# Optimization experiments

Measured on AMD Instinct MI355X. Metric: run time of the kernel, lower is better.

## Reference

```python
import jax, jax.numpy as jnp
import numpy as np

B, N, M = 256, 2048, 128          # batch, memory rows, memory word size
VEC, H, E = 256, 1024, 512        # vector_length, hidden_size, embed_dim
SHIFTS = 3                        # shift kernel size {-1,0,+1}
P = M + 3 + SHIFTS                # k(M), beta(1), g(1), s(3), gamma(1)
EPS = 1e-16


def _xavier(k, shape):
    fan_out, fan_in = shape
    lim = float(np.sqrt(6.0 / (fan_in + fan_out)))
    return jax.random.uniform(k, shape, jnp.float32, -lim, lim)


def setup_inputs() -> dict:
    key = jax.random.key(0)
    ks = jax.random.split(key, 16)
    x = jax.random.normal(ks[0], (B, VEC + M), jnp.float32)
    memory = jax.random.normal(ks[1], (B, N, M), jnp.float32) * 0.1
    prev_read_w = jax.nn.softmax(jax.random.normal(ks[2], (B, N), jnp.float32), axis=1)
    prev_write_w = jax.nn.softmax(jax.random.normal(ks[3], (B, N), jnp.float32), axis=1)
    h_prev = jax.random.normal(ks[4], (B, H), jnp.float32) * 0.1
    c_prev = jax.random.normal(ks[5], (B, H), jnp.float32) * 0.1
    # LSTM controller params (torch gate order i,f,g,o)
    W_ih = _xavier(ks[6], (4 * H, VEC + M))
    W_hh = _xavier(ks[7], (4 * H, H))
    b_ih = jnp.zeros((4 * H,), jnp.float32)
    b_hh = jnp.zeros((4 * H,), jnp.float32)
    # read head fc: hidden -> k,beta,g,s,gamma
    W_r = _xavier(ks[8], (P, H)); b_r = jnp.zeros((P,), jnp.float32)
    # write head fc: hidden -> k,beta,g,s,gamma,e(M),a(M)
    W_w = _xavier(ks[9], (P + 2 * M, H)); b_w = jnp.zeros((P + 2 * M,), jnp.float32)
    # output fc: (hidden + M) -> embed_dim
    W_fc = _xavier(ks[10], (E, H + M))
    b_fc = jax.random.normal(ks[11], (E,), jnp.float32) * 0.01
    return dict(x=x, memory=memory, prev_read_w=prev_read_w, prev_write_w=prev_write_w,
                h_prev=h_prev, c_prev=c_prev, W_ih=W_ih, W_hh=W_hh, b_ih=b_ih, b_hh=b_hh,
                W_r=W_r, b_r=b_r, W_w=W_w, b_w=b_w, W_fc=W_fc, b_fc=b_fc)


def _address(p, memory, prev_w):
    # p: [B, P] raw head parameters; memory: [B,N,M]; prev_w: [B,N]
    k = jnp.tanh(p[:, :M])                                   # [B,M]
    beta = jax.nn.softplus(p[:, M:M + 1])                    # [B,1]
    g = jax.nn.sigmoid(p[:, M + 1:M + 2])                    # [B,1]
    s = jax.nn.softmax(p[:, M + 2:M + 2 + SHIFTS], axis=1)   # [B,3]
    gamma = 1.0 + jax.nn.softplus(p[:, M + 2 + SHIFTS:P])    # [B,1]
    # content addressing: cosine similarity * beta -> softmax over N
    dot = jnp.einsum('bnm,bm->bn', memory, k)
    denom = jnp.linalg.norm(memory, axis=-1) * jnp.linalg.norm(k, axis=-1, keepdims=True) + EPS
    w_c = jax.nn.softmax(beta * (dot / denom), axis=1)
    # gated interpolation with previous weights
    w_g = g * w_c + (1.0 - g) * prev_w
    # circular convolution with 3-tap shift kernel
    w_t = (s[:, 0:1] * jnp.roll(w_g, 1, axis=1)
           + s[:, 1:2] * w_g
           + s[:, 2:3] * jnp.roll(w_g, -1, axis=1))
    # sharpening
    w_p = w_t ** gamma
    return w_p / (jnp.sum(w_p, axis=1, keepdims=True) + EPS)


def reference(x, memory, prev_read_w, prev_write_w, h_prev, c_prev,
              W_ih, W_hh, b_ih, b_hh, W_r, b_r, W_w, b_w, W_fc, b_fc):
    # LSTM controller step
    gates = x @ W_ih.T + b_ih + h_prev @ W_hh.T + b_hh
    i, f, gg, o = jnp.split(gates, 4, axis=1)
    c = jax.nn.sigmoid(f) * c_prev + jax.nn.sigmoid(i) * jnp.tanh(gg)
    h = jax.nn.sigmoid(o) * jnp.tanh(c)                       # controller output [B,H]
    # read head: address then read
    w_r = _address(h @ W_r.T + b_r, memory, prev_read_w)
    read = jnp.einsum('bn,bnm->bm', w_r, memory)              # [B,M]
    # write head: address then erase/add
    wp = h @ W_w.T + b_w
    w_w = _address(wp[:, :P], memory, prev_write_w)
    e = jax.nn.sigmoid(wp[:, P:P + M])                        # erase [B,M]
    a = jnp.tanh(wp[:, P + M:P + 2 * M])                      # add   [B,M]
    new_memory = memory * (1.0 - w_w[:, :, None] * e[:, None, :]) + w_w[:, :, None] * a[:, None, :]
    # output
    out = jax.nn.sigmoid(jnp.concatenate([h, read], axis=1) @ W_fc.T + b_fc)  # [B,E]
    return out, new_memory
```

## Files before the change

kernel.cpp:

```cpp
#include <hip/hip_runtime.h>
#include <hip/hip_bf16.h>

#define B_    256
#define N_    2048
#define M_    128
#define VEC_  256
#define H_    1024
#define E_    512
#define P_    134
#define XDIM  384
#define G4H   4096
#define PWC   524

typedef float  floatx4  __attribute__((ext_vector_type(4)));
typedef short  bf16x8   __attribute__((ext_vector_type(8)));
typedef unsigned short ushortx8 __attribute__((ext_vector_type(8)));
typedef unsigned short ushortx4 __attribute__((ext_vector_type(4)));

#define OFF_GATES 0
#define OFF_H     (OFF_GATES + B_*G4H)
#define OFF_PW    (OFF_H     + B_*H_)
#define OFF_KR    (OFF_PW    + B_*PWC)
#define OFF_KW    (OFF_KR    + B_*M_)
#define OFF_E     (OFF_KW    + B_*M_)
#define OFF_A     (OFF_E     + B_*M_)
#define OFF_SCAL  (OFF_A     + B_*M_)
#define OFF_DOTR  (OFF_SCAL  + B_*16)
#define OFF_DOTW  (OFF_DOTR  + B_*N_)
#define OFF_MNORM (OFF_DOTW  + B_*N_)
#define OFF_WR    (OFF_MNORM + B_*N_)
#define OFF_WW    (OFF_WR    + B_*N_)
#define OFF_READ  (OFF_WW    + B_*N_)
#define FLOAT_TOTAL (OFF_READ + B_*M_)
#define SOFF_X    0
#define SOFF_H    (SOFF_X   + B_*XDIM)
#define SOFF_WIH  (SOFF_H   + B_*H_)
#define SOFF_WHH  (SOFF_WIH + G4H*XDIM)
#define SHORT_TOTAL (SOFF_WHH + G4H*H_)

__device__ __forceinline__ float bf2f(unsigned short u) {
    return __uint_as_float(((unsigned int)u) << 16);
}
__device__ __forceinline__ unsigned short f2bf(float f) {
    unsigned int x = __float_as_uint(f);
    x += 0x7fffu + ((x >> 16) & 1u);
    return (unsigned short)(x >> 16);
}
__device__ __forceinline__ float sigm(float x) { return 1.f / (1.f + expf(-x)); }
__device__ __forceinline__ float softplus_(float x) { return x > 20.f ? x : log1pf(expf(x)); }

__global__ __launch_bounds__(256) void k_cvt4(
    const float* __restrict__ s0, const float* __restrict__ s1,
    const float* __restrict__ s2, const float* __restrict__ s3,
    unsigned short* __restrict__ dst)
{
    int i = (blockIdx.x * 256 + threadIdx.x) * 4;
    const float* s; int off;
    if      (i < SOFF_H)    { s = s0; off = SOFF_X; }
    else if (i < SOFF_WIH)  { s = s1; off = SOFF_H; }
    else if (i < SOFF_WHH)  { s = s2; off = SOFF_WIH; }
    else                    { s = s3; off = SOFF_WHH; }
    floatx4 v = *(const floatx4*)(s + (i - off));
    ushortx4 o;
    o[0] = f2bf(v[0]); o[1] = f2bf(v[1]); o[2] = f2bf(v[2]); o[3] = f2bf(v[3]);
    *(ushortx4*)(dst + i) = o;
}

__global__ __launch_bounds__(256) void k_gates(
    const unsigned short* __restrict__ wsb,
    const float* __restrict__ b_ih, const float* __restrict__ b_hh,
    float* __restrict__ gates)
{
    const unsigned short* x      = wsb + SOFF_X;
    const unsigned short* h_prev = wsb + SOFF_H;
    const unsigned short* W_ih   = wsb + SOFF_WIH;
    const unsigned short* W_hh   = wsb + SOFF_WHH;

    int gtid  = blockIdx.x * 256 + threadIdx.x;
    int wid   = gtid >> 6;
    int lane  = threadIdx.x & 63;
    int tileM = wid >> 7;
    int nGrp  = wid & 127;
    int m0 = tileM << 4, n0 = nGrp << 5;
    int quad = lane >> 4, r16 = lane & 15;
    int koff = quad << 3;
    int mA = m0 + r16;

    floatx4 acc[2];
#pragma unroll
    for (int s = 0; s < 2; ++s) acc[s] = (floatx4){0.f, 0.f, 0.f, 0.f};

    const unsigned short* xrow = x + mA * XDIM;
    const unsigned short* hrow = h_prev + mA * H_;

#pragma unroll 4
    for (int kk = 0; kk < 12; ++kk) {
        int k = (kk << 5) + koff;
        bf16x8 a  = *(const bf16x8*)(xrow + k);
        bf16x8 b0 = *(const bf16x8*)(W_ih + (n0 +  0 + r16) * XDIM + k);
        bf16x8 b1 = *(const bf16x8*)(W_ih + (n0 + 16 + r16) * XDIM + k);
        acc[0] = __builtin_amdgcn_mfma_f32_16x16x32_bf16(a, b0, acc[0], 0, 0, 0);
        acc[1] = __builtin_amdgcn_mfma_f32_16x16x32_bf16(a, b1, acc[1], 0, 0, 0);
    }
#pragma unroll 4
    for (int kk = 0; kk < 32; ++kk) {
        int k = (kk << 5) + koff;
        bf16x8 a  = *(const bf16x8*)(hrow + k);
        bf16x8 b0 = *(const bf16x8*)(W_hh + (n0 +  0 + r16) * H_ + k);
        bf16x8 b1 = *(const bf16x8*)(W_hh + (n0 + 16 + r16) * H_ + k);
        acc[0] = __builtin_amdgcn_mfma_f32_16x16x32_bf16(a, b0, acc[0], 0, 0, 0);
        acc[1] = __builtin_amdgcn_mfma_f32_16x16x32_bf16(a, b1, acc[1], 0, 0, 0);
    }
#pragma unroll
    for (int s = 0; s < 2; ++s) {
        int n = n0 + (s << 4) + r16;
        float bias = b_ih[n] + b_hh[n];
#pragma unroll
        for (int r = 0; r < 4; ++r) {
            int m = m0 + (quad << 2) + r;
            gates[m * G4H + n] = acc[s][r] + bias;
        }
    }
}

__global__ __launch_bounds__(256) void k_ctrl(
    const float* __restrict__ gates, const float* __restrict__ c_prev,
    const float* __restrict__ W_r, const float* __restrict__ b_r,
    const float* __restrict__ W_w, const float* __restrict__ b_w,
    float* __restrict__ h_out,
    float* __restrict__ kr, float* __restrict__ kw,
    float* __restrict__ e,  float* __restrict__ a,
    float* __restrict__ scal, float* __restrict__ read_acc)
{
    __shared__ __align__(16) float hs[H_];
    __shared__ __align__(16) float pws[PWC];
    __shared__ float red[8];
    int b = blockIdx.x, t = threadIdx.x;
    const float* g = gates + (size_t)b * G4H;

#pragma unroll
    for (int jj = 0; jj < 4; ++jj) {
        int j = t + (jj << 8);
        float ig = sigm(g[j]);
        float fg = sigm(g[1024 + j]);
        float gg = tanhf(g[2048 + j]);
        float og = sigm(g[3072 + j]);
        float c  = fg * c_prev[b * H_ + j] + ig * gg;
        float hv = og * tanhf(c);
        hs[j] = hv;
        h_out[b * H_ + j] = hv;
    }
    __syncthreads();

    int c0 = t, c1 = t + 256, c2v = (t < 12);
    const float* w0; float bias0;
    if (c0 < P_) { w0 = W_r + c0 * H_; bias0 = b_r[c0]; }
    else         { w0 = W_w + (c0 - P_) * H_; bias0 = b_w[c0 - P_]; }
    const float* w1 = W_w + (c1 - P_) * H_;
    float bias1 = b_w[c1 - P_];
    const float* w2 = W_w + (c2v ? (t + 512 - P_) : 0) * H_;
    float acc0 = 0.f, acc1 = 0.f, acc2 = 0.f;
#pragma unroll 4
    for (int k = 0; k < H_; k += 4) {
        floatx4 hv = *(const floatx4*)&hs[k];
        floatx4 a0 = *(const floatx4*)(w0 + k);
        floatx4 a1 = *(const floatx4*)(w1 + k);
        floatx4 a2 = *(const floatx4*)(w2 + k);
#pragma unroll
        for (int j = 0; j < 4; ++j) {
            acc0 = fmaf(a0[j], hv[j], acc0);
            acc1 = fmaf(a1[j], hv[j], acc1);
            acc2 = fmaf(a2[j], hv[j], acc2);
        }
    }
    pws[c0] = acc0 + bias0;
    pws[c1] = acc1 + bias1;
    if (c2v) pws[t + 512] = acc2 + b_w[t + 512 - P_];
    __syncthreads();

    float krv = 0.f, kwv = 0.f;
    if (t < 128) {
        krv = tanhf(pws[t]);
        kwv = tanhf(pws[P_ + t]);
        kr[b * M_ + t] = krv;
        kw[b * M_ + t] = kwv;
        e [b * M_ + t] = sigm (pws[268 + t]);
        a [b * M_ + t] = tanhf(pws[396 + t]);
        read_acc[b * M_ + t] = 0.f;
    }
    float sr = krv * krv, sw = kwv * kwv;
#pragma unroll
    for (int m = 32; m; m >>= 1) { sr += __shfl_xor(sr, m); sw += __shfl_xor(sw, m); }
    if ((t & 63) == 0) { red[(t >> 6) * 2] = sr; red[(t >> 6) * 2 + 1] = sw; }
    __syncthreads();
    if (t == 0) {
        float nr = sqrtf(red[0] + red[2] + red[4] + red[6]);
        float nw = sqrtf(red[1] + red[3] + red[5] + red[7]);
        float* sc = scal + b * 16;
        {
            float beta = softplus_(pws[128]);
            float gg   = sigm(pws[129]);
            float s0 = pws[130], s1 = pws[131], s2 = pws[132];
            float mx = fmaxf(s0, fmaxf(s1, s2));
            float e0 = expf(s0 - mx), e1 = expf(s1 - mx), e2 = expf(s2 - mx);
            float es = e0 + e1 + e2;
            sc[0] = beta; sc[1] = gg; sc[2] = e0 / es; sc[3] = e1 / es; sc[4] = e2 / es;
            sc[5] = 1.f + softplus_(pws[133]); sc[6] = nr;
        }
        {
            float beta = softplus_(pws[262]);
            float gg   = sigm(pws[263]);
            float s0 = pws[264], s1 = pws[265], s2 = pws[266];
            float mx = fmaxf(s0, fmaxf(s1, s2));
            float e0 = expf(s0 - mx), e1 = expf(s1 - mx), e2 = expf(s2 - mx);
            float es = e0 + e1 + e2;
            sc[8] = beta; sc[9] = gg; sc[10] = e0 / es; sc[11] = e1 / es; sc[12] = e2 / es;
            sc[13] = 1.f + softplus_(pws[267]); sc[14] = nw;
        }
    }
}

__global__ __launch_bounds__(256) void k_pass1(
    const float* __restrict__ memory,
    const float* __restrict__ kr, const float* __restrict__ kw,
    float* __restrict__ dotr, float* __restrict__ dotw, float* __restrict__ mnorm)
{
    int b = blockIdx.x >> 4;
    int chunk = blockIdx.x & 15;
    __shared__ __align__(16) float krs[M_], kws[M_];
    int t = threadIdx.x;
    if (t < 128) krs[t] = kr[b * M_ + t];
    else         kws[t - 128] = kw[b * M_ + t - 128];
    __syncthreads();
    int wave = t >> 6, lane = t & 63;
    int col  = (lane & 31) << 2;
    int half = lane >> 5;
    floatx4 kr4 = *(const floatx4*)&krs[col];
    floatx4 kw4 = *(const floatx4*)&kws[col];
    int rowbase = chunk * 128 + wave * 32;
#pragma unroll 4
    for (int i = 0; i < 16; ++i) {
        int n = rowbase + (i << 1) + half;
        size_t ro = (size_t)b * N_ + n;
        floatx4 mv = __builtin_nontemporal_load((const floatx4*)(memory + ro * M_ + col));
        float dr = mv[0] * kr4[0] + mv[1] * kr4[1] + mv[2] * kr4[2] + mv[3] * kr4[3];
        float dw = mv[0] * kw4[0] + mv[1] * kw4[1] + mv[2] * kw4[2] + mv[3] * kw4[3];
        float ss = mv[0] * mv[0] + mv[1] * mv[1] + mv[2] * mv[2] + mv[3] * mv[3];
#pragma unroll
        for (int m = 16; m; m >>= 1) {
            dr += __shfl_xor(dr, m);
            dw += __shfl_xor(dw, m);
            ss += __shfl_xor(ss, m);
        }
        if ((lane & 31) == 0) {
            dotr[ro] = dr; dotw[ro] = dw; mnorm[ro] = sqrtf(ss);
        }
    }
}

__device__ __forceinline__ float blkSum(float v, float* red) {
#pragma unroll
    for (int m = 32; m; m >>= 1) v += __shfl_xor(v, m);
    int w = threadIdx.x >> 6;
    if ((threadIdx.x & 63) == 0) red[w] = v;
    __syncthreads();
    float r = red[0] + red[1] + red[2] + red[3];
    __syncthreads();
    return r;
}
__device__ __forceinline__ float blkMax(float v, float* red) {
#pragma unroll
    for (int m = 32; m; m >>= 1) v = fmaxf(v, __shfl_xor(v, m));
    int w = threadIdx.x >> 6;
    if ((threadIdx.x & 63) == 0) red[w] = v;
    __syncthreads();
    float r = fmaxf(fmaxf(red[0], red[1]), fmaxf(red[2], red[3]));
    __syncthreads();
    return r;
}

__global__ __launch_bounds__(256) void k_address(
    const float* __restrict__ dotr, const float* __restrict__ dotw,
    const float* __restrict__ mnorm,
    const float* __restrict__ prev_r, const float* __restrict__ prev_w,
    const float* __restrict__ scal,
    float* __restrict__ wr, float* __restrict__ ww)
{
    int b = blockIdx.x >> 1, head = blockIdx.x & 1;
    const float* dot = head ? dotw : dotr;
    const float* prev = head ? prev_w : prev_r;
    float* wout = head ? ww : wr;
    const float* sc = scal + b * 16 + head * 8;
    float beta = sc[0], g = sc[1], s0 = sc[2], s1 = sc[3], s2 = sc[4];
    float gamma = sc[5], kn = sc[6];

    __shared__ float buf[N_];
    __shared__ float red[4];
    int t = threadIdx.x;
    size_t base = (size_t)b * N_;

    float loc[8];
    float mx = -1e30f;
#pragma unroll
    for (int i = 0; i < 8; ++i) {
        int n = (i << 8) + t;
        float xv = beta * dot[base + n] / (mnorm[base + n] * kn + 1e-16f);
        loc[i] = xv;
        mx = fmaxf(mx, xv);
    }
    mx = blkMax(mx, red);
    float sum = 0.f;
#pragma unroll
    for (int i = 0; i < 8; ++i) { float ev = expf(loc[i] - mx); loc[i] = ev; sum += ev; }
    sum = blkSum(sum, red);
    float inv = 1.f / sum;
#pragma unroll
    for (int i = 0; i < 8; ++i) {
        int n = (i << 8) + t;
        float wc = loc[i] * inv;
        buf[n] = g * wc + (1.f - g) * prev[base + n];
    }
    __syncthreads();
    float psum = 0.f;
#pragma unroll
    for (int i = 0; i < 8; ++i) {
        int n = (i << 8) + t;
        float wt = s0 * buf[(n + N_ - 1) & (N_ - 1)] + s1 * buf[n] + s2 * buf[(n + 1) & (N_ - 1)];
        float wp = powf(wt, gamma);
        loc[i] = wp;
        psum += wp;
    }
    psum = blkSum(psum, red);
    float invp = 1.f / (psum + 1e-16f);
#pragma unroll
    for (int i = 0; i < 8; ++i) {
        int n = (i << 8) + t;
        wout[base + n] = loc[i] * invp;
    }
}

__global__ __launch_bounds__(256) void k_update(
    const float* __restrict__ memory,
    const float* __restrict__ wr, const float* __restrict__ ww,
    const float* __restrict__ e, const float* __restrict__ a,
    float* __restrict__ read_acc,
    float* __restrict__ newmem)
{
    int b = blockIdx.x >> 5;
    int chunk = blockIdx.x & 31;
    int t = threadIdx.x;
    __shared__ float es[M_], as_[M_];
    if (t < 128) es[t] = e[b * M_ + t];
    else         as_[t - 128] = a[b * M_ + t - 128];
    __syncthreads();

    int c = t & 15, r = t >> 4;
    int m8 = c << 3;
    float ev[8], av[8], racc[8];
#pragma unroll
    for (int j = 0; j < 8; ++j) { ev[j] = es[m8 + j]; av[j] = as_[m8 + j]; racc[j] = 0.f; }

#pragma unroll
    for (int stp = 0; stp < 4; ++stp) {
        int n = chunk * 64 + stp * 16 + r;
        size_t ro = (size_t)b * N_ + n;
        floatx4 mv0 = __builtin_nontemporal_load((const floatx4*)(memory + ro * M_ + m8));
        floatx4 mv1 = __builtin_nontemporal_load((const floatx4*)(memory + ro * M_ + m8 + 4));
        float wwv = ww[ro], wrv = wr[ro];
        floatx4 o0, o1;
#pragma unroll
        for (int j = 0; j < 4; ++j) {
            float mf = mv0[j];
            o0[j] = mf * (1.f - wwv * ev[j]) + wwv * av[j];
            racc[j] = fmaf(wrv, mf, racc[j]);
        }
#pragma unroll
        for (int j = 0; j < 4; ++j) {
            float mf = mv1[j];
            o1[j] = mf * (1.f - wwv * ev[4 + j]) + wwv * av[4 + j];
            racc[4 + j] = fmaf(wrv, mf, racc[4 + j]);
        }
        __builtin_nontemporal_store(o0, (floatx4*)(newmem + ro * M_ + m8));
        __builtin_nontemporal_store(o1, (floatx4*)(newmem + ro * M_ + m8 + 4));
    }

    __shared__ float rbuf[16][M_];
#pragma unroll
    for (int j = 0; j < 8; ++j) rbuf[r][m8 + j] = racc[j];
    __syncthreads();
    if (t < 128) {
        float s = 0.f;
#pragma unroll
        for (int rr = 0; rr < 16; ++rr) s += rbuf[rr][t];
        atomicAdd(read_acc + b * M_ + t, s);
    }
}

__global__ __launch_bounds__(256) void k_out(
    const float* __restrict__ h, const float* __restrict__ read_acc,
    const float* __restrict__ W_fc, const float* __restrict__ b_fc,
    float* __restrict__ out)
{
    __shared__ __align__(16) float hc[H_ + M_];
    int b = blockIdx.x, t = threadIdx.x;
    for (int i = t; i < H_; i += 256) hc[i] = h[b * H_ + i];
    if (t < 128) hc[H_ + t] = read_acc[b * M_ + t];
    __syncthreads();
    int c0 = t, c1 = t + 256;
    const float* w0 = W_fc + c0 * (H_ + M_);
    const float* w1 = W_fc + c1 * (H_ + M_);
    float acc0 = 0.f, acc1 = 0.f;
#pragma unroll 4
    for (int k = 0; k < H_ + M_; k += 4) {
        floatx4 hv = *(const floatx4*)&hc[k];
        floatx4 a0 = *(const floatx4*)(w0 + k);
        floatx4 a1 = *(const floatx4*)(w1 + k);
#pragma unroll
        for (int j = 0; j < 4; ++j) {
            acc0 = fmaf(a0[j], hv[j], acc0);
            acc1 = fmaf(a1[j], hv[j], acc1);
        }
    }
    out[b * E_ + c0] = sigm(acc0 + b_fc[c0]);
    out[b * E_ + c1] = sigm(acc1 + b_fc[c1]);
}

extern "C" void kernel_launch(void* const* d_in, const int* in_sizes, int n_in,
                              void* d_out, int out_size, void* d_ws, size_t ws_size,
                              hipStream_t stream)
{
    (void)in_sizes; (void)n_in; (void)out_size; (void)ws_size;
    const float* x      = (const float*)d_in[0];
    const float* memory = (const float*)d_in[1];
    const float* prev_r = (const float*)d_in[2];
    const float* prev_w = (const float*)d_in[3];
    const float* h_prev = (const float*)d_in[4];
    const float* c_prev = (const float*)d_in[5];
    const float* W_ih   = (const float*)d_in[6];
    const float* W_hh   = (const float*)d_in[7];
    const float* b_ih   = (const float*)d_in[8];
    const float* b_hh   = (const float*)d_in[9];
    const float* W_r    = (const float*)d_in[10];
    const float* b_r    = (const float*)d_in[11];
    const float* W_w    = (const float*)d_in[12];
    const float* b_w    = (const float*)d_in[13];
    const float* W_fc   = (const float*)d_in[14];
    const float* b_fc   = (const float*)d_in[15];

    float* ws = (float*)d_ws;
    float* gates = ws + OFF_GATES;
    float* h     = ws + OFF_H;
    float* kr    = ws + OFF_KR;
    float* kw    = ws + OFF_KW;
    float* e     = ws + OFF_E;
    float* a     = ws + OFF_A;
    float* scal  = ws + OFF_SCAL;
    float* dotr  = ws + OFF_DOTR;
    float* dotw  = ws + OFF_DOTW;
    float* mnorm = ws + OFF_MNORM;
    float* wrb   = ws + OFF_WR;
    float* wwb   = ws + OFF_WW;
    float* rd    = ws + OFF_READ;
    unsigned short* wsb = (unsigned short*)(ws + FLOAT_TOTAL);

    float* out    = (float*)d_out;
    float* newmem = out + B_ * E_;

    k_cvt4   <<<SHORT_TOTAL / 1024, 256, 0, stream>>>(x, h_prev, W_ih, W_hh, wsb);
    k_gates  <<<512,   256, 0, stream>>>(wsb, b_ih, b_hh, gates);
    k_ctrl   <<<256,   256, 0, stream>>>(gates, c_prev, W_r, b_r, W_w, b_w,
                                         h, kr, kw, e, a, scal, rd);
    k_pass1  <<<4096,  256, 0, stream>>>(memory, kr, kw, dotr, dotw, mnorm);
    k_address<<<512,   256, 0, stream>>>(dotr, dotw, mnorm, prev_r, prev_w, scal, wrb, wwb);
    k_update <<<8192,  256, 0, stream>>>(memory, wrb, wwb, e, a, rd, newmem);
    k_out    <<<256,   256, 0, stream>>>(h, rd, W_fc, b_fc, out);
}
```

Before: 771.4 us.

## Fuse weight bf16 conversion into gates GEMM and replace read atomics with partials

The gates kernel now converts its slice of W_ih/W_hh to bf16 straight into swizzled LDS, so the separate full-weight conversion pass and its round trip through workspace go away. Each block then reuses that B tile across four M tiles. The memory pass swaps shuffle reductions for DPP adds and drops nontemporal loads, aiming for L2 reuse of memory between the pass1 and update kernels. The update kernel runs blocks in reverse order, doubles the rows per block, and writes per-chunk read partials instead of atomics. The output kernel reduces those partials and splits the columns across two blocks per batch. Addressing uses fast exp and pow intrinsics, which slightly changes precision.

```diff
diff --git a/kernel.cpp b/kernel.cpp
--- a/kernel.cpp
+++ b/kernel.cpp
@@ -19,8 +19,7 @@
 
 #define OFF_GATES 0
 #define OFF_H     (OFF_GATES + B_*G4H)
-#define OFF_PW    (OFF_H     + B_*H_)
-#define OFF_KR    (OFF_PW    + B_*PWC)
+#define OFF_KR    (OFF_H     + B_*H_)
 #define OFF_KW    (OFF_KR    + B_*M_)
 #define OFF_E     (OFF_KW    + B_*M_)
 #define OFF_A     (OFF_E     + B_*M_)
@@ -30,17 +29,12 @@
 #define OFF_MNORM (OFF_DOTW  + B_*N_)
 #define OFF_WR    (OFF_MNORM + B_*N_)
 #define OFF_WW    (OFF_WR    + B_*N_)
-#define OFF_READ  (OFF_WW    + B_*N_)
-#define FLOAT_TOTAL (OFF_READ + B_*M_)
+#define OFF_RDP   (OFF_WW    + B_*N_)
+#define FLOAT_TOTAL (OFF_RDP + B_*16*M_)
 #define SOFF_X    0
 #define SOFF_H    (SOFF_X   + B_*XDIM)
-#define SOFF_WIH  (SOFF_H   + B_*H_)
-#define SOFF_WHH  (SOFF_WIH + G4H*XDIM)
-#define SHORT_TOTAL (SOFF_WHH + G4H*H_)
-
-__device__ __forceinline__ float bf2f(unsigned short u) {
-    return __uint_as_float(((unsigned int)u) << 16);
-}
+#define SHORT_TOTAL (SOFF_H + B_*H_)
+
 __device__ __forceinline__ unsigned short f2bf(float f) {
     unsigned int x = __float_as_uint(f);
     x += 0x7fffu + ((x >> 16) & 1u);
@@ -49,17 +43,17 @@
 __device__ __forceinline__ float sigm(float x) { return 1.f / (1.f + expf(-x)); }
 __device__ __forceinline__ float softplus_(float x) { return x > 20.f ? x : log1pf(expf(x)); }
 
-__global__ __launch_bounds__(256) void k_cvt4(
-    const float* __restrict__ s0, const float* __restrict__ s1,
-    const float* __restrict__ s2, const float* __restrict__ s3,
+#define DPP_ADD(v, ctrl) \
+    v += __int_as_float(__builtin_amdgcn_update_dpp(0, __float_as_int(v), ctrl, 0xF, 0xF, true))
+
+__global__ __launch_bounds__(256) void k_cvt2(
+    const float* __restrict__ x, const float* __restrict__ h,
     unsigned short* __restrict__ dst)
 {
     int i = (blockIdx.x * 256 + threadIdx.x) * 4;
     const float* s; int off;
-    if      (i < SOFF_H)    { s = s0; off = SOFF_X; }
-    else if (i < SOFF_WIH)  { s = s1; off = SOFF_H; }
-    else if (i < SOFF_WHH)  { s = s2; off = SOFF_WIH; }
-    else                    { s = s3; off = SOFF_WHH; }
+    if (i < SOFF_H) { s = x; off = SOFF_X; }
+    else            { s = h; off = SOFF_H; }
     floatx4 v = *(const floatx4*)(s + (i - off));
     ushortx4 o;
     o[0] = f2bf(v[0]); o[1] = f2bf(v[1]); o[2] = f2bf(v[2]); o[3] = f2bf(v[3]);
@@ -68,58 +62,83 @@
 
 __global__ __launch_bounds__(256) void k_gates(
     const unsigned short* __restrict__ wsb,
+    const float* __restrict__ W_ih, const float* __restrict__ W_hh,
     const float* __restrict__ b_ih, const float* __restrict__ b_hh,
     float* __restrict__ gates)
 {
-    const unsigned short* x      = wsb + SOFF_X;
-    const unsigned short* h_prev = wsb + SOFF_H;
-    const unsigned short* W_ih   = wsb + SOFF_WIH;
-    const unsigned short* W_hh   = wsb + SOFF_WHH;
-
-    int gtid  = blockIdx.x * 256 + threadIdx.x;
-    int wid   = gtid >> 6;
-    int lane  = threadIdx.x & 63;
-    int tileM = wid >> 7;
-    int nGrp  = wid & 127;
-    int m0 = tileM << 4, n0 = nGrp << 5;
+    __shared__ unsigned short Bp[16 * 1408];
+    char* Bb = (char*)Bp;
+    const unsigned short* xb = wsb + SOFF_X;
+    const unsigned short* hb = wsb + SOFF_H;
+
+    int n0 = blockIdx.x << 4;
+    int t  = threadIdx.x;
+
+#pragma unroll
+    for (int it = 0; it < 11; ++it) {
+        int j   = it * 256 + t;
+        int row = j / 176;
+        int co8 = (j - row * 176) * 8;
+        const float* src = (co8 < 384)
+            ? (W_ih + (size_t)(n0 + row) * XDIM + co8)
+            : (W_hh + (size_t)(n0 + row) * H_ + (co8 - 384));
+        floatx4 f0 = *(const floatx4*)src;
+        floatx4 f1 = *(const floatx4*)(src + 4);
+        ushortx8 o;
+        o[0] = f2bf(f0[0]); o[1] = f2bf(f0[1]); o[2] = f2bf(f0[2]); o[3] = f2bf(f0[3]);
+        o[4] = f2bf(f1[0]); o[5] = f2bf(f1[1]); o[6] = f2bf(f1[2]); o[7] = f2bf(f1[3]);
+        int kb  = co8 * 2;
+        int dst = row * 2816 + (kb ^ ((row & 7) << 4));
+        *(ushortx8*)(Bb + dst) = o;
+    }
+    __syncthreads();
+
+    int w    = t >> 6;
+    int lane = t & 63;
     int quad = lane >> 4, r16 = lane & 15;
-    int koff = quad << 3;
-    int mA = m0 + r16;
-
-    floatx4 acc[2];
-#pragma unroll
-    for (int s = 0; s < 2; ++s) acc[s] = (floatx4){0.f, 0.f, 0.f, 0.f};
-
-    const unsigned short* xrow = x + mA * XDIM;
-    const unsigned short* hrow = h_prev + mA * H_;
+    int swz  = (r16 & 7) << 4;
+    const char* Brow = Bb + r16 * 2816;
+
+    const unsigned short* xr[4];
+    const unsigned short* hr[4];
+#pragma unroll
+    for (int mi = 0; mi < 4; ++mi) {
+        int mA = ((w << 2) + mi) * 16 + r16;
+        xr[mi] = xb + mA * XDIM;
+        hr[mi] = hb + mA * H_;
+    }
+    floatx4 acc[4];
+#pragma unroll
+    for (int mi = 0; mi < 4; ++mi) acc[mi] = (floatx4){0.f, 0.f, 0.f, 0.f};
 
 #pragma unroll 4
     for (int kk = 0; kk < 12; ++kk) {
-        int k = (kk << 5) + koff;
-        bf16x8 a  = *(const bf16x8*)(xrow + k);
-        bf16x8 b0 = *(const bf16x8*)(W_ih + (n0 +  0 + r16) * XDIM + k);
-        bf16x8 b1 = *(const bf16x8*)(W_ih + (n0 + 16 + r16) * XDIM + k);
-        acc[0] = __builtin_amdgcn_mfma_f32_16x16x32_bf16(a, b0, acc[0], 0, 0, 0);
-        acc[1] = __builtin_amdgcn_mfma_f32_16x16x32_bf16(a, b1, acc[1], 0, 0, 0);
+        int k0 = (kk << 5) + (quad << 3);
+        bf16x8 b = *(const bf16x8*)(Brow + (((kk << 6) + (quad << 4)) ^ swz));
+#pragma unroll
+        for (int mi = 0; mi < 4; ++mi) {
+            bf16x8 a = *(const bf16x8*)(xr[mi] + k0);
+            acc[mi] = __builtin_amdgcn_mfma_f32_16x16x32_bf16(a, b, acc[mi], 0, 0, 0);
+        }
     }
 #pragma unroll 4
     for (int kk = 0; kk < 32; ++kk) {
-        int k = (kk << 5) + koff;
-        bf16x8 a  = *(const bf16x8*)(hrow + k);
-        bf16x8 b0 = *(const bf16x8*)(W_hh + (n0 +  0 + r16) * H_ + k);
-        bf16x8 b1 = *(const bf16x8*)(W_hh + (n0 + 16 + r16) * H_ + k);
-        acc[0] = __builtin_amdgcn_mfma_f32_16x16x32_bf16(a, b0, acc[0], 0, 0, 0);
-        acc[1] = __builtin_amdgcn_mfma_f32_16x16x32_bf16(a, b1, acc[1], 0, 0, 0);
-    }
-#pragma unroll
-    for (int s = 0; s < 2; ++s) {
-        int n = n0 + (s << 4) + r16;
-        float bias = b_ih[n] + b_hh[n];
-#pragma unroll
-        for (int r = 0; r < 4; ++r) {
-            int m = m0 + (quad << 2) + r;
-            gates[m * G4H + n] = acc[s][r] + bias;
-        }
+        int k0 = (kk << 5) + (quad << 3);
+        bf16x8 b = *(const bf16x8*)(Brow + ((768 + (kk << 6) + (quad << 4)) ^ swz));
+#pragma unroll
+        for (int mi = 0; mi < 4; ++mi) {
+            bf16x8 a = *(const bf16x8*)(hr[mi] + k0);
+            acc[mi] = __builtin_amdgcn_mfma_f32_16x16x32_bf16(a, b, acc[mi], 0, 0, 0);
+        }
+    }
+    int n = n0 + r16;
+    float bias = b_ih[n] + b_hh[n];
+#pragma unroll
+    for (int mi = 0; mi < 4; ++mi) {
+        int mbase = ((w << 2) + mi) * 16 + (quad << 2);
+#pragma unroll
+        for (int r = 0; r < 4; ++r)
+            gates[(mbase + r) * G4H + n] = acc[mi][r] + bias;
     }
 }
 
@@ -130,7 +149,7 @@
     float* __restrict__ h_out,
     float* __restrict__ kr, float* __restrict__ kw,
     float* __restrict__ e,  float* __restrict__ a,
-    float* __restrict__ scal, float* __restrict__ read_acc)
+    float* __restrict__ scal)
 {
     __shared__ __align__(16) float hs[H_];
     __shared__ __align__(16) float pws[PWC];
@@ -186,7 +205,6 @@
         kw[b * M_ + t] = kwv;
         e [b * M_ + t] = sigm (pws[268 + t]);
         a [b * M_ + t] = tanhf(pws[396 + t]);
-        read_acc[b * M_ + t] = 0.f;
     }
     float sr = krv * krv, sw = kwv * kwv;
 #pragma unroll
@@ -242,16 +260,17 @@
     for (int i = 0; i < 16; ++i) {
         int n = rowbase + (i << 1) + half;
         size_t ro = (size_t)b * N_ + n;
-        floatx4 mv = __builtin_nontemporal_load((const floatx4*)(memory + ro * M_ + col));
+        floatx4 mv = *(const floatx4*)(memory + ro * M_ + col);
         float dr = mv[0] * kr4[0] + mv[1] * kr4[1] + mv[2] * kr4[2] + mv[3] * kr4[3];
         float dw = mv[0] * kw4[0] + mv[1] * kw4[1] + mv[2] * kw4[2] + mv[3] * kw4[3];
         float ss = mv[0] * mv[0] + mv[1] * mv[1] + mv[2] * mv[2] + mv[3] * mv[3];
-#pragma unroll
-        for (int m = 16; m; m >>= 1) {
-            dr += __shfl_xor(dr, m);
-            dw += __shfl_xor(dw, m);
-            ss += __shfl_xor(ss, m);
-        }
+        DPP_ADD(dr, 0x128); DPP_ADD(dw, 0x128); DPP_ADD(ss, 0x128);
+        DPP_ADD(dr, 0x124); DPP_ADD(dw, 0x124); DPP_ADD(ss, 0x124);
+        DPP_ADD(dr, 0x122); DPP_ADD(dw, 0x122); DPP_ADD(ss, 0x122);
+        DPP_ADD(dr, 0x121); DPP_ADD(dw, 0x121); DPP_ADD(ss, 0x121);
+        dr += __shfl_xor(dr, 16);
+        dw += __shfl_xor(dw, 16);
+        ss += __shfl_xor(ss, 16);
         if ((lane & 31) == 0) {
             dotr[ro] = dr; dotw[ro] = dw; mnorm[ro] = sqrtf(ss);
         }
@@ -311,7 +330,7 @@
     mx = blkMax(mx, red);
     float sum = 0.f;
 #pragma unroll
-    for (int i = 0; i < 8; ++i) { float ev = expf(loc[i] - mx); loc[i] = ev; sum += ev; }
+    for (int i = 0; i < 8; ++i) { float ev = __expf(loc[i] - mx); loc[i] = ev; sum += ev; }
     sum = blkSum(sum, red);
     float inv = 1.f / sum;
 #pragma unroll
@@ -326,7 +345,7 @@
     for (int i = 0; i < 8; ++i) {
         int n = (i << 8) + t;
         float wt = s0 * buf[(n + N_ - 1) & (N_ - 1)] + s1 * buf[n] + s2 * buf[(n + 1) & (N_ - 1)];
-        float wp = powf(wt, gamma);
+        float wp = __powf(wt, gamma);
         loc[i] = wp;
         psum += wp;
     }
@@ -343,11 +362,12 @@
     const float* __restrict__ memory,
     const float* __restrict__ wr, const float* __restrict__ ww,
     const float* __restrict__ e, const float* __restrict__ a,
-    float* __restrict__ read_acc,
+    float* __restrict__ rd_part,
     float* __restrict__ newmem)
 {
-    int b = blockIdx.x >> 5;
-    int chunk = blockIdx.x & 31;
+    int j = 4095 - (int)blockIdx.x;
+    int b = j >> 4;
+    int chunk = j & 15;
     int t = threadIdx.x;
     __shared__ float es[M_], as_[M_];
     if (t < 128) es[t] = e[b * M_ + t];
@@ -358,27 +378,27 @@
     int m8 = c << 3;
     float ev[8], av[8], racc[8];
 #pragma unroll
-    for (int j = 0; j < 8; ++j) { ev[j] = es[m8 + j]; av[j] = as_[m8 + j]; racc[j] = 0.f; }
-
-#pragma unroll
-    for (int stp = 0; stp < 4; ++stp) {
-        int n = chunk * 64 + stp * 16 + r;
+    for (int jj = 0; jj < 8; ++jj) { ev[jj] = es[m8 + jj]; av[jj] = as_[m8 + jj]; racc[jj] = 0.f; }
+
+#pragma unroll
+    for (int stp = 0; stp < 8; ++stp) {
+        int n = chunk * 128 + stp * 16 + r;
         size_t ro = (size_t)b * N_ + n;
-        floatx4 mv0 = __builtin_nontemporal_load((const floatx4*)(memory + ro * M_ + m8));
-        floatx4 mv1 = __builtin_nontemporal_load((const floatx4*)(memory + ro * M_ + m8 + 4));
+        floatx4 mv0 = *(const floatx4*)(memory + ro * M_ + m8);
+        floatx4 mv1 = *(const floatx4*)(memory + ro * M_ + m8 + 4);
         float wwv = ww[ro], wrv = wr[ro];
         floatx4 o0, o1;
 #pragma unroll
-        for (int j = 0; j < 4; ++j) {
-            float mf = mv0[j];
-            o0[j] = mf * (1.f - wwv * ev[j]) + wwv * av[j];
-            racc[j] = fmaf(wrv, mf, racc[j]);
-        }
-#pragma unroll
-        for (int j = 0; j < 4; ++j) {
-            float mf = mv1[j];
-            o1[j] = mf * (1.f - wwv * ev[4 + j]) + wwv * av[4 + j];
-            racc[4 + j] = fmaf(wrv, mf, racc[4 + j]);
+        for (int jj = 0; jj < 4; ++jj) {
+            float mf = mv0[jj];
+            o0[jj] = mf * (1.f - wwv * ev[jj]) + wwv * av[jj];
+            racc[jj] = fmaf(wrv, mf, racc[jj]);
+        }
+#pragma unroll
+        for (int jj = 0; jj < 4; ++jj) {
+            float mf = mv1[jj];
+            o1[jj] = mf * (1.f - wwv * ev[4 + jj]) + wwv * av[4 + jj];
+            racc[4 + jj] = fmaf(wrv, mf, racc[4 + jj]);
         }
         __builtin_nontemporal_store(o0, (floatx4*)(newmem + ro * M_ + m8));
         __builtin_nontemporal_store(o1, (floatx4*)(newmem + ro * M_ + m8 + 4));
@@ -386,43 +406,48 @@
 
     __shared__ float rbuf[16][M_];
 #pragma unroll
-    for (int j = 0; j < 8; ++j) rbuf[r][m8 + j] = racc[j];
+    for (int jj = 0; jj < 8; ++jj) rbuf[r][m8 + jj] = racc[jj];
     __syncthreads();
     if (t < 128) {
         float s = 0.f;
 #pragma unroll
         for (int rr = 0; rr < 16; ++rr) s += rbuf[rr][t];
-        atomicAdd(read_acc + b * M_ + t, s);
+        rd_part[((b << 4) + chunk) * M_ + t] = s;
     }
 }
 
 __global__ __launch_bounds__(256) void k_out(
-    const float* __restrict__ h, const float* __restrict__ read_acc,
+    const float* __restrict__ h, const float* __restrict__ rd_part,
     const float* __restrict__ W_fc, const float* __restrict__ b_fc,
     float* __restrict__ out)
 {
     __shared__ __align__(16) float hc[H_ + M_];
-    int b = blockIdx.x, t = threadIdx.x;
+    int b = blockIdx.x >> 1, half = blockIdx.x & 1;
+    int t = threadIdx.x;
     for (int i = t; i < H_; i += 256) hc[i] = h[b * H_ + i];
-    if (t < 128) hc[H_ + t] = read_acc[b * M_ + t];
-    __syncthreads();
-    int c0 = t, c1 = t + 256;
-    const float* w0 = W_fc + c0 * (H_ + M_);
-    const float* w1 = W_fc + c1 * (H_ + M_);
+    if (t < 128) {
+        float s = 0.f;
+#pragma unroll
+        for (int p = 0; p < 16; ++p) s += rd_part[((b << 4) + p) * M_ + t];
+        hc[H_ + t] = s;
+    }
+    __syncthreads();
+    int c = half * 256 + t;
+    const float* wrow = W_fc + c * (H_ + M_);
     float acc0 = 0.f, acc1 = 0.f;
 #pragma unroll 4
-    for (int k = 0; k < H_ + M_; k += 4) {
-        floatx4 hv = *(const floatx4*)&hc[k];
-        floatx4 a0 = *(const floatx4*)(w0 + k);
-        floatx4 a1 = *(const floatx4*)(w1 + k);
-#pragma unroll
-        for (int j = 0; j < 4; ++j) {
-            acc0 = fmaf(a0[j], hv[j], acc0);
-            acc1 = fmaf(a1[j], hv[j], acc1);
-        }
-    }
-    out[b * E_ + c0] = sigm(acc0 + b_fc[c0]);
-    out[b * E_ + c1] = sigm(acc1 + b_fc[c1]);
+    for (int k = 0; k < H_ + M_; k += 8) {
+        floatx4 w0 = *(const floatx4*)(wrow + k);
+        floatx4 w1 = *(const floatx4*)(wrow + k + 4);
+        floatx4 h0 = *(const floatx4*)&hc[k];
+        floatx4 h1 = *(const floatx4*)&hc[k + 4];
+#pragma unroll
+        for (int jj = 0; jj < 4; ++jj) {
+            acc0 = fmaf(w0[jj], h0[jj], acc0);
+            acc1 = fmaf(w1[jj], h1[jj], acc1);
+        }
+    }
+    out[b * E_ + c] = sigm(acc0 + acc1 + b_fc[c]);
 }
 
 extern "C" void kernel_launch(void* const* d_in, const int* in_sizes, int n_in,
@@ -460,18 +485,18 @@
     float* mnorm = ws + OFF_MNORM;
     float* wrb   = ws + OFF_WR;
     float* wwb   = ws + OFF_WW;
-    float* rd    = ws + OFF_READ;
+    float* rdp   = ws + OFF_RDP;
     unsigned short* wsb = (unsigned short*)(ws + FLOAT_TOTAL);
 
     float* out    = (float*)d_out;
     float* newmem = out + B_ * E_;
 
-    k_cvt4   <<<SHORT_TOTAL / 1024, 256, 0, stream>>>(x, h_prev, W_ih, W_hh, wsb);
-    k_gates  <<<512,   256, 0, stream>>>(wsb, b_ih, b_hh, gates);
+    k_cvt2   <<<SHORT_TOTAL / 1024, 256, 0, stream>>>(x, h_prev, wsb);
+    k_gates  <<<256,   256, 0, stream>>>(wsb, W_ih, W_hh, b_ih, b_hh, gates);
     k_ctrl   <<<256,   256, 0, stream>>>(gates, c_prev, W_r, b_r, W_w, b_w,
-                                         h, kr, kw, e, a, scal, rd);
+                                         h, kr, kw, e, a, scal);
     k_pass1  <<<4096,  256, 0, stream>>>(memory, kr, kw, dotr, dotw, mnorm);
     k_address<<<512,   256, 0, stream>>>(dotr, dotw, mnorm, prev_r, prev_w, scal, wrb, wwb);
-    k_update <<<8192,  256, 0, stream>>>(memory, wrb, wwb, e, a, rd, newmem);
-    k_out    <<<256,   256, 0, stream>>>(h, rd, W_fc, b_fc, out);
-}
+    k_update <<<4096,  256, 0, stream>>>(memory, wrb, wwb, e, a, rdp, newmem);
+    k_out    <<<512,   256, 0, stream>>>(h, rdp, W_fc, b_fc, out);
+}
```

Measured after the change: 721.7 us. 6.4% less time.
